# Kernel tuning notes

Measured on AMD Instinct MI355X. Metric: run time of the kernel, lower is better.

The kernel has to match this reference:

```python
import jax, jax.numpy as jnp
import numpy as np


def _l2_normalize(x, eps=1e-12):
    # matches torch.nn.functional.normalize(p=2, dim=-1)
    n = jnp.linalg.norm(x, axis=-1, keepdims=True)
    return x / jnp.maximum(n, eps)


def setup_inputs() -> dict:
    key = jax.random.key(0)
    kq, kk, kv = jax.random.split(key, 3)
    B, H, N, D = 4, 12, 8192, 64
    Q = jax.random.normal(kq, (B, H, N, D), dtype=jnp.float32)
    K = jax.random.normal(kk, (B, H, N, D), dtype=jnp.float32)
    V = jax.random.normal(kv, (B, H, N, D), dtype=jnp.float32)
    mask = jnp.ones((B, N), dtype=jnp.float32)
    return {"Q": Q, "K": K, "V": V, "mask": mask}


def reference(Q, K, V, mask):
    N = Q.shape[2]
    scale = 1.0 / np.sqrt(np.sqrt(N)).astype(np.float32)  # N^{-1/4}
    m = mask[:, None, :, None]                 # [B,1,N,1]
    Qf = _l2_normalize(Q) * scale              # [B,H,N,D]
    Kf = _l2_normalize(K) * m * scale          # [B,H,N,D]
    Vm = V * m                                 # [B,H,N,D]
    # linear attention: (K^T V) is [B,H,D,D], then Q @ (K^T V)
    KtV = jnp.einsum('bhnd,bhne->bhde', Kf, Vm)
    return jnp.einsum('bhnd,bhde->bhne', Qf, KtV)
```

## Files before the change

kernel.cpp:

```cpp
#include <hip/hip_runtime.h>
#include <cmath>

#define Bn 4
#define Hn 12
#define BH 48
#define Nn 8192
#define Dn 64

typedef float f32x4 __attribute__((ext_vector_type(4)));
typedef short bf16x8 __attribute__((ext_vector_type(8)));

__device__ __forceinline__ int swz(int d) { return ((d >> 2) & 7) << 3; }

__device__ __forceinline__ unsigned cvt_pk_bf16(float lo, float hi) {
    unsigned r;
    asm("v_cvt_pk_bf16_f32 %0, %1, %2" : "=v"(r) : "v"(lo), "v"(hi));
    return r;
}

__global__ __launch_bounds__(256) void ktv_kernel(
    const float* __restrict__ K, const float* __restrict__ V,
    const float* __restrict__ mask, float* __restrict__ partial,
    float scale, int ch)
{
    const int chunk = blockIdx.x, head = blockIdx.y;
    const int bb = head / Hn;
    const int rowsPer = Nn / ch;
    const int n0 = chunk * rowsPer;
    const float* Kp = K + ((size_t)head * Nn + n0) * Dn;
    const float* Vp = V + ((size_t)head * Nn + n0) * Dn;
    const float* mp = mask + (size_t)bb * Nn + n0;

    __shared__ __align__(16) ushort sKT[64 * 64];
    __shared__ __align__(16) ushort sVT[64 * 64];

    const int t = threadIdx.x;
    const int w = t >> 6, l = t & 63;
    const int g = t >> 4;
    const int c4 = (t & 15) << 2;

    f32x4 acc[4] = {{0.f,0.f,0.f,0.f},{0.f,0.f,0.f,0.f},
                    {0.f,0.f,0.f,0.f},{0.f,0.f,0.f,0.f}};

    float4 kr[4], vr[4];
    float mk[4];
    #pragma unroll
    for (int s = 0; s < 4; ++s) {
        kr[s] = *(const float4*)(Kp + (size_t)(4*g + s) * Dn + c4);
        vr[s] = *(const float4*)(Vp + (size_t)(4*g + s) * Dn + c4);
        mk[s] = mp[4*g + s];
    }

    const int ntiles = rowsPer >> 6;
    for (int tt = 0; tt < ntiles; ++tt) {
        float rf[4];
        #pragma unroll
        for (int s = 0; s < 4; ++s) {
            float ss = kr[s].x*kr[s].x + kr[s].y*kr[s].y
                     + kr[s].z*kr[s].z + kr[s].w*kr[s].w;
            #pragma unroll
            for (int off = 1; off < 16; off <<= 1) ss += __shfl_xor(ss, off, 64);
            rf[s] = scale * mk[s] * mk[s] / fmaxf(sqrtf(ss), 1e-12f);
        }

        __syncthreads();
        const float* krf = (const float*)kr;
        const float* vrf = (const float*)vr;
        #pragma unroll
        for (int j = 0; j < 4; ++j) {
            const int d = c4 + j;
            const int base = d * 64;
            const int sw = swz(d);
            const int p0 = (4*g)     ^ sw;
            const int p2 = (4*g + 2) ^ sw;
            *(unsigned*)&sKT[base + p0] = cvt_pk_bf16(krf[j]     * rf[0], krf[4+j]  * rf[1]);
            *(unsigned*)&sKT[base + p2] = cvt_pk_bf16(krf[8+j]   * rf[2], krf[12+j] * rf[3]);
            *(unsigned*)&sVT[base + p0] = cvt_pk_bf16(vrf[j],            vrf[4+j]);
            *(unsigned*)&sVT[base + p2] = cvt_pk_bf16(vrf[8+j],          vrf[12+j]);
        }
        __syncthreads();

        if (tt + 1 < ntiles) {
            const float* Kn = Kp + (size_t)(tt + 1) * 64 * Dn;
            const float* Vn = Vp + (size_t)(tt + 1) * 64 * Dn;
            #pragma unroll
            for (int s = 0; s < 4; ++s) {
                kr[s] = *(const float4*)(Kn + (size_t)(4*g + s) * Dn + c4);
                vr[s] = *(const float4*)(Vn + (size_t)(4*g + s) * Dn + c4);
                mk[s] = mp[(tt + 1) * 64 + 4*g + s];
            }
        }

        const int e   = (w << 4) + (l & 15);
        const int nsl = (l >> 4) << 3;
        const int swe = swz(e);
        #pragma unroll
        for (int h = 0; h < 2; ++h) {
            const bf16x8 a = *(const bf16x8*)&sVT[e * 64 + ((h*32 + nsl) ^ swe)];
            #pragma unroll
            for (int P = 0; P < 4; ++P) {
                const int d = (P << 4) + (l & 15);
                const bf16x8 bq = *(const bf16x8*)&sKT[d * 64 + ((h*32 + nsl) ^ swz(d))];
                acc[P] = __builtin_amdgcn_mfma_f32_16x16x32_bf16(a, bq, acc[P], 0, 0, 0);
            }
        }
    }

    float* pp = partial + (size_t)(head * ch + chunk) * (Dn * Dn);
    #pragma unroll
    for (int P = 0; P < 4; ++P)
        #pragma unroll
        for (int r = 0; r < 4; ++r)
            pp[((w << 4) + ((l >> 4) << 2) + r) * 64 + (P << 4) + (l & 15)] = acc[P][r];
}

__global__ __launch_bounds__(256) void ktv_reduce_kernel(
    const float* __restrict__ partial, ushort* __restrict__ ktvT, int ch)
{
    const int head = blockIdx.y;
    const int e = blockIdx.x * 256 + threadIdx.x;
    const float* pp = partial + (size_t)head * ch * (Dn * Dn) + e;
    float s = 0.f;
    for (int c = 0; c < ch; ++c) s += pp[(size_t)c * (Dn * Dn)];
    unsigned u = __float_as_uint(s);
    u = (u + 0x7fffu + ((u >> 16) & 1u)) >> 16;
    ktvT[(size_t)head * (Dn * Dn) + e] = (ushort)u;
}

__global__ __launch_bounds__(256) void qktv_kernel(
    const float* __restrict__ Q, const ushort* __restrict__ ktvT,
    float* __restrict__ out, float scale)
{
    const int chunk = blockIdx.x, head = blockIdx.y;
    const int n0 = chunk * (Nn / 16);
    const float* Qp = Q + ((size_t)head * Nn + n0) * Dn;
    float* Op = out + ((size_t)head * Nn + n0) * Dn;
    const ushort* kp = ktvT + (size_t)head * (Dn * Dn);

    const int t = threadIdx.x, w = t >> 6, l = t & 63;
    const int lr = l & 15;
    const int lg = l >> 4;

    bf16x8 bf[4][2];
    #pragma unroll
    for (int E = 0; E < 4; ++E)
        #pragma unroll
        for (int h = 0; h < 2; ++h)
            bf[E][h] = *(const bf16x8*)&kp[(16 * E + lr) * 64 + 32 * h + 8 * lg];

    for (int i = 0; i < 8; ++i) {
        const int strip = i * 4 + w;
        const float* qrow = Qp + (size_t)(strip * 16 + lr) * Dn;
        const float4 f0 = *(const float4*)(qrow + 8 * lg);
        const float4 f1 = *(const float4*)(qrow + 8 * lg + 4);
        const float4 f2 = *(const float4*)(qrow + 32 + 8 * lg);
        const float4 f3 = *(const float4*)(qrow + 32 + 8 * lg + 4);

        float ss = f0.x*f0.x + f0.y*f0.y + f0.z*f0.z + f0.w*f0.w
                 + f1.x*f1.x + f1.y*f1.y + f1.z*f1.z + f1.w*f1.w
                 + f2.x*f2.x + f2.y*f2.y + f2.z*f2.z + f2.w*f2.w
                 + f3.x*f3.x + f3.y*f3.y + f3.z*f3.z + f3.w*f3.w;
        ss += __shfl_xor(ss, 16, 64);
        ss += __shfl_xor(ss, 32, 64);
        const float inv = scale / fmaxf(sqrtf(ss), 1e-12f);

        union { unsigned u[4]; bf16x8 v; } a0, a1;
        a0.u[0] = cvt_pk_bf16(f0.x*inv, f0.y*inv);
        a0.u[1] = cvt_pk_bf16(f0.z*inv, f0.w*inv);
        a0.u[2] = cvt_pk_bf16(f1.x*inv, f1.y*inv);
        a0.u[3] = cvt_pk_bf16(f1.z*inv, f1.w*inv);
        a1.u[0] = cvt_pk_bf16(f2.x*inv, f2.y*inv);
        a1.u[1] = cvt_pk_bf16(f2.z*inv, f2.w*inv);
        a1.u[2] = cvt_pk_bf16(f3.x*inv, f3.y*inv);
        a1.u[3] = cvt_pk_bf16(f3.z*inv, f3.w*inv);

        #pragma unroll
        for (int E = 0; E < 4; ++E) {
            f32x4 c = {0.f, 0.f, 0.f, 0.f};
            c = __builtin_amdgcn_mfma_f32_16x16x32_bf16(a0.v, bf[E][0], c, 0, 0, 0);
            c = __builtin_amdgcn_mfma_f32_16x16x32_bf16(a1.v, bf[E][1], c, 0, 0, 0);
            #pragma unroll
            for (int r = 0; r < 4; ++r)
                Op[(size_t)(strip * 16 + 4 * lg + r) * Dn + 16 * E + lr] = c[r];
        }
    }
}

extern "C" void kernel_launch(void* const* d_in, const int* in_sizes, int n_in,
                              void* d_out, int out_size, void* d_ws, size_t ws_size,
                              hipStream_t stream)
{
    const float* Q    = (const float*)d_in[0];
    const float* K    = (const float*)d_in[1];
    const float* V    = (const float*)d_in[2];
    const float* mask = (const float*)d_in[3];
    float* out = (float*)d_out;

    const float scale = 1.0f / sqrtf(sqrtf((float)Nn));

    const size_t KTV_BYTES = (size_t)BH * Dn * Dn * sizeof(ushort);
    int ch = 64;
    while (ch > 1 &&
           KTV_BYTES + (size_t)BH * ch * Dn * Dn * 4 > ws_size)
        ch >>= 1;

    ushort* ktvT   = (ushort*)d_ws;
    float* partial = (float*)((char*)d_ws + KTV_BYTES);

    ktv_kernel<<<dim3(ch, BH), 256, 0, stream>>>(K, V, mask, partial, scale, ch);
    ktv_reduce_kernel<<<dim3((Dn * Dn) / 256, BH), 256, 0, stream>>>(partial, ktvT, ch);
    qktv_kernel<<<dim3(16, BH), 256, 0, stream>>>(Q, ktvT, out, scale);
}
```

Baseline: 115.6 us.

## Process two 64-row tiles per iteration in ktv kernel and cut chunk count

The K^T V kernel now loads, normalizes and stages two 64-row tiles into double-sized shared buffers per loop iteration, halving the number of barrier pairs and doubling the bytes in flight per prefetch. The chunk count per head drops from 64 to 16, so each block covers more rows and the partial buffer and reduction shrink. The trade-offs are a grid of only 768 blocks, more registers for the doubled prefetch, and twice the shared memory, all of which may lower occupancy.

```diff
diff --git a/kernel.cpp b/kernel.cpp
--- a/kernel.cpp
+++ b/kernel.cpp
@@ -31,8 +31,8 @@
     const float* Vp = V + ((size_t)head * Nn + n0) * Dn;
     const float* mp = mask + (size_t)bb * Nn + n0;
 
-    __shared__ __align__(16) ushort sKT[64 * 64];
-    __shared__ __align__(16) ushort sVT[64 * 64];
+    __shared__ __align__(16) ushort sKT[2][64 * 64];
+    __shared__ __align__(16) ushort sVT[2][64 * 64];
 
     const int t = threadIdx.x;
     const int w = t >> 6, l = t & 63;
@@ -42,76 +42,87 @@
     f32x4 acc[4] = {{0.f,0.f,0.f,0.f},{0.f,0.f,0.f,0.f},
                     {0.f,0.f,0.f,0.f},{0.f,0.f,0.f,0.f}};
 
-    float4 kr[4], vr[4];
-    float mk[4];
+    float4 kr[2][4], vr[2][4];
+    float mk[2][4];
     #pragma unroll
-    for (int s = 0; s < 4; ++s) {
-        kr[s] = *(const float4*)(Kp + (size_t)(4*g + s) * Dn + c4);
-        vr[s] = *(const float4*)(Vp + (size_t)(4*g + s) * Dn + c4);
-        mk[s] = mp[4*g + s];
-    }
-
-    const int ntiles = rowsPer >> 6;
-    for (int tt = 0; tt < ntiles; ++tt) {
-        float rf[4];
+    for (int hh = 0; hh < 2; ++hh)
         #pragma unroll
         for (int s = 0; s < 4; ++s) {
-            float ss = kr[s].x*kr[s].x + kr[s].y*kr[s].y
-                     + kr[s].z*kr[s].z + kr[s].w*kr[s].w;
-            #pragma unroll
-            for (int off = 1; off < 16; off <<= 1) ss += __shfl_xor(ss, off, 64);
-            rf[s] = scale * mk[s] * mk[s] / fmaxf(sqrtf(ss), 1e-12f);
-        }
+            kr[hh][s] = *(const float4*)(Kp + (size_t)(hh * 64 + 4*g + s) * Dn + c4);
+            vr[hh][s] = *(const float4*)(Vp + (size_t)(hh * 64 + 4*g + s) * Dn + c4);
+            mk[hh][s] = mp[hh * 64 + 4*g + s];
+        }
+
+    const int nper = rowsPer >> 7;
+    for (int pp = 0; pp < nper; ++pp) {
+        float rf[2][4];
+        #pragma unroll
+        for (int hh = 0; hh < 2; ++hh)
+            #pragma unroll
+            for (int s = 0; s < 4; ++s) {
+                float ss = kr[hh][s].x*kr[hh][s].x + kr[hh][s].y*kr[hh][s].y
+                         + kr[hh][s].z*kr[hh][s].z + kr[hh][s].w*kr[hh][s].w;
+                #pragma unroll
+                for (int off = 1; off < 16; off <<= 1) ss += __shfl_xor(ss, off, 64);
+                rf[hh][s] = scale * mk[hh][s] * mk[hh][s] / fmaxf(sqrtf(ss), 1e-12f);
+            }
 
         __syncthreads();
-        const float* krf = (const float*)kr;
-        const float* vrf = (const float*)vr;
-        #pragma unroll
-        for (int j = 0; j < 4; ++j) {
-            const int d = c4 + j;
-            const int base = d * 64;
-            const int sw = swz(d);
-            const int p0 = (4*g)     ^ sw;
-            const int p2 = (4*g + 2) ^ sw;
-            *(unsigned*)&sKT[base + p0] = cvt_pk_bf16(krf[j]     * rf[0], krf[4+j]  * rf[1]);
-            *(unsigned*)&sKT[base + p2] = cvt_pk_bf16(krf[8+j]   * rf[2], krf[12+j] * rf[3]);
-            *(unsigned*)&sVT[base + p0] = cvt_pk_bf16(vrf[j],            vrf[4+j]);
-            *(unsigned*)&sVT[base + p2] = cvt_pk_bf16(vrf[8+j],          vrf[12+j]);
+        #pragma unroll
+        for (int hh = 0; hh < 2; ++hh) {
+            const float* krf = (const float*)kr[hh];
+            const float* vrf = (const float*)vr[hh];
+            #pragma unroll
+            for (int j = 0; j < 4; ++j) {
+                const int d = c4 + j;
+                const int base = d * 64;
+                const int sw = swz(d);
+                const int p0 = (4*g)     ^ sw;
+                const int p2 = (4*g + 2) ^ sw;
+                *(unsigned*)&sKT[hh][base + p0] = cvt_pk_bf16(krf[j]     * rf[hh][0], krf[4+j]  * rf[hh][1]);
+                *(unsigned*)&sKT[hh][base + p2] = cvt_pk_bf16(krf[8+j]   * rf[hh][2], krf[12+j] * rf[hh][3]);
+                *(unsigned*)&sVT[hh][base + p0] = cvt_pk_bf16(vrf[j],            vrf[4+j]);
+                *(unsigned*)&sVT[hh][base + p2] = cvt_pk_bf16(vrf[8+j],          vrf[12+j]);
+            }
         }
         __syncthreads();
 
-        if (tt + 1 < ntiles) {
-            const float* Kn = Kp + (size_t)(tt + 1) * 64 * Dn;
-            const float* Vn = Vp + (size_t)(tt + 1) * 64 * Dn;
-            #pragma unroll
-            for (int s = 0; s < 4; ++s) {
-                kr[s] = *(const float4*)(Kn + (size_t)(4*g + s) * Dn + c4);
-                vr[s] = *(const float4*)(Vn + (size_t)(4*g + s) * Dn + c4);
-                mk[s] = mp[(tt + 1) * 64 + 4*g + s];
-            }
+        if (pp + 1 < nper) {
+            const float* Kn = Kp + (size_t)(pp + 1) * 128 * Dn;
+            const float* Vn = Vp + (size_t)(pp + 1) * 128 * Dn;
+            #pragma unroll
+            for (int hh = 0; hh < 2; ++hh)
+                #pragma unroll
+                for (int s = 0; s < 4; ++s) {
+                    kr[hh][s] = *(const float4*)(Kn + (size_t)(hh * 64 + 4*g + s) * Dn + c4);
+                    vr[hh][s] = *(const float4*)(Vn + (size_t)(hh * 64 + 4*g + s) * Dn + c4);
+                    mk[hh][s] = mp[(pp + 1) * 128 + hh * 64 + 4*g + s];
+                }
         }
 
         const int e   = (w << 4) + (l & 15);
         const int nsl = (l >> 4) << 3;
         const int swe = swz(e);
         #pragma unroll
-        for (int h = 0; h < 2; ++h) {
-            const bf16x8 a = *(const bf16x8*)&sVT[e * 64 + ((h*32 + nsl) ^ swe)];
-            #pragma unroll
-            for (int P = 0; P < 4; ++P) {
-                const int d = (P << 4) + (l & 15);
-                const bf16x8 bq = *(const bf16x8*)&sKT[d * 64 + ((h*32 + nsl) ^ swz(d))];
-                acc[P] = __builtin_amdgcn_mfma_f32_16x16x32_bf16(a, bq, acc[P], 0, 0, 0);
+        for (int hh = 0; hh < 2; ++hh)
+            #pragma unroll
+            for (int h = 0; h < 2; ++h) {
+                const bf16x8 a = *(const bf16x8*)&sVT[hh][e * 64 + ((h*32 + nsl) ^ swe)];
+                #pragma unroll
+                for (int P = 0; P < 4; ++P) {
+                    const int d = (P << 4) + (l & 15);
+                    const bf16x8 bq = *(const bf16x8*)&sKT[hh][d * 64 + ((h*32 + nsl) ^ swz(d))];
+                    acc[P] = __builtin_amdgcn_mfma_f32_16x16x32_bf16(a, bq, acc[P], 0, 0, 0);
+                }
             }
-        }
     }
 
-    float* pp = partial + (size_t)(head * ch + chunk) * (Dn * Dn);
+    float* pp2 = partial + (size_t)(head * ch + chunk) * (Dn * Dn);
     #pragma unroll
     for (int P = 0; P < 4; ++P)
         #pragma unroll
         for (int r = 0; r < 4; ++r)
-            pp[((w << 4) + ((l >> 4) << 2) + r) * 64 + (P << 4) + (l & 15)] = acc[P][r];
+            pp2[((w << 4) + ((l >> 4) << 2) + r) * 64 + (P << 4) + (l & 15)] = acc[P][r];
 }
 
 __global__ __launch_bounds__(256) void ktv_reduce_kernel(
@@ -199,7 +210,7 @@
     const float scale = 1.0f / sqrtf(sqrtf((float)Nn));
 
     const size_t KTV_BYTES = (size_t)BH * Dn * Dn * sizeof(ushort);
-    int ch = 64;
+    int ch = 16;
     while (ch > 1 &&
            KTV_BYTES + (size_t)BH * ch * Dn * Dn * 4 > ws_size)
         ch >>= 1;
```

Result: faster. 101.2 us (-12.4%).
